# Kernel tuning notes

Measured on AMD Instinct MI355X. Metric: run time of the kernel, lower is better.

Reference implementation:

```python
import jax, jax.numpy as jnp
import numpy as np

PATCH_SIZES = (2, 4, 6, 8)
KERNEL_SIZES = (3, 5, 7)
K_FREQ = 1
K_ROUTE = 3


def setup_inputs():
    key = jax.random.key(0)
    ks = iter(jax.random.split(key, 40))
    B, T, N, D, dt = 8, 1024, 32, 128, 128
    P = len(PATCH_SIZES)
    def rn(shape, s=0.02):
        return jax.random.normal(next(ks), shape, jnp.float32) * s
    inp = {
        'z': jax.random.normal(next(ks), (B, T, N, D), jnp.float32),
        'noise_feat': jax.random.normal(next(ks), (B * N, T, D), jnp.float32),
        'noise_logits': jax.random.normal(next(ks), (B * N, T, P), jnp.float32),
        'Wq_tr': rn((D, len(KERNEL_SIZES))), 'bq_tr': jnp.zeros((len(KERNEL_SIZES),), jnp.float32),
        'Wf': rn((3 * D, D)), 'bf': jnp.zeros((D,), jnp.float32),
        'Wr': rn((D, P)), 'br': jnp.zeros((P,), jnp.float32),
        'Wn': rn((D, P)), 'bn': jnp.zeros((P,), jnp.float32),
        'local_qkv_w': rn((P, 3, D, dt)), 'local_qkv_b': jnp.zeros((P, 3, dt), jnp.float32),
        'gqkv_b': jnp.zeros((P, 3, dt), jnp.float32),
        'proj_w': rn((P, dt, D)), 'proj_b': jnp.zeros((P, D), jnp.float32),
        'conv_b': jnp.zeros((P, D), jnp.float32),
    }
    for p in PATCH_SIZES:
        inp['gqkv_w_p%d' % p] = rn((3, p * D, dt))
        inp['conv_w_p%d' % p] = rn((D, D, p))
    return inp


def _forward(z, noise_feat, noise_logits, Wq_tr, bq_tr, Wf, bf, Wr, br, Wn, bn,
             local_qkv_w, local_qkv_b, gqkv_w_p2, gqkv_w_p4, gqkv_w_p6, gqkv_w_p8,
             gqkv_b, proj_w, proj_b, conv_w_p2, conv_w_p4, conv_w_p6, conv_w_p8, conv_b):
    B, T, N, D = z.shape
    BN = B * N
    dt = proj_w.shape[1]
    P = len(PATCH_SIZES)
    zf = z.transpose(0, 2, 1, 3).reshape(BN, T, D)  # (BN, T, D)

    # --- DFT seasonal extractor: keep top-K_FREQ magnitude frequencies per (series, channel)
    zfft = jnp.fft.rfft(zf, axis=1)                 # (BN, F, D) complex
    mag = jnp.abs(zfft).astype(jnp.float32)
    Fr = mag.shape[1]
    magT = mag.transpose(0, 2, 1)                   # (BN, D, F)
    vals, idx = jax.lax.top_k(magT, K_FREQ)
    oh = (idx[..., None] == jnp.arange(Fr)).astype(jnp.float32)  # (BN, D, k, F)
    maskT = (oh * vals[..., None]).sum(axis=2)      # scatter top-k magnitudes
    factor = (maskT / (magT + 1e-8)).transpose(0, 2, 1)
    z_sea = jnp.fft.irfft(zfft * factor, n=T, axis=1).astype(zf.dtype)
    z_rem = zf - z_sea

    # --- multi-scale trend (avg_pool1d, count_include_pad=True, stride 1, pad k//2)
    alpha = jax.nn.softmax(z_rem.mean(axis=1) @ Wq_tr + bq_tr, axis=-1)  # (BN, n_k)
    def avg_pool(x, k):
        pd = k // 2
        xp = jnp.pad(x, ((0, 0), (pd, pd), (0, 0)))
        cs = jnp.pad(jnp.cumsum(xp, axis=1), ((0, 0), (1, 0), (0, 0)))
        return (cs[:, k:] - cs[:, :-k]) / k          # length T for odd k
    pooled = jnp.stack([avg_pool(z_rem, k) for k in KERNEL_SIZES], axis=1)  # (BN, n_k, T, D)
    z_trend = jnp.einsum('bk,bktd->btd', alpha, pooled)

    # --- noisy top-k gating router
    z_fused = jnp.concatenate([zf, z_sea, z_trend], axis=-1) @ Wf + bf
    gating = z_fused + noise_feat * 0.1
    logits = gating @ Wr + br + noise_logits * jax.nn.softplus(gating @ Wn + bn)
    rw = jax.nn.softmax(logits, axis=-1)            # (BN, T, P)
    tv, ti = jax.lax.top_k(rw, K_ROUTE)
    sparse = ((ti[..., None] == jnp.arange(P)).astype(rw.dtype) * tv[..., None]).sum(axis=2)

    # --- per-patch-size dual attention branches
    gqkv_ws = (gqkv_w_p2, gqkv_w_p4, gqkv_w_p6, gqkv_w_p8)
    conv_ws = (conv_w_p2, conv_w_p4, conv_w_p6, conv_w_p8)
    scale = dt ** -0.5
    out = jnp.zeros((BN, D, T), jnp.float32)
    for i, p in enumerate(PATCH_SIZES):
        pad = (-T) % p
        zp = jnp.pad(zf, ((0, 0), (0, pad), (0, 0)))
        Np = (T + pad) // p
        patches = zp.reshape(BN, Np, p, D)
        # local attention: patch-mean query against patch elements
        lw, lb = local_qkv_w[i], local_qkv_b[i]
        q = patches.mean(axis=2) @ lw[0] + lb[0]                   # (BN, Np, dt)
        kk = jnp.einsum('bnpd,de->bnpe', patches, lw[1]) + lb[1]
        vv = jnp.einsum('bnpd,de->bnpe', patches, lw[2]) + lb[2]
        la = jax.nn.softmax(jnp.einsum('bne,bnpe->bnp', q, kk) * scale, axis=-1)
        local_out = jnp.einsum('bnp,bnpe->bne', la, vv)
        # global attention over flattened patches (sigmoid THEN scale THEN softmax, as in source)
        flat = patches.reshape(BN, Np, p * D)
        gw, gb = gqkv_ws[i], gqkv_b[i]
        gq = flat @ gw[0] + gb[0]
        gk = flat @ gw[1] + gb[1]
        gv = flat @ gw[2] + gb[2]
        ga = jax.nn.softmax(jax.nn.sigmoid(jnp.einsum('bme,bne->bmn', gq, gk)) * scale, axis=-1)
        global_out = jnp.einsum('bmn,bne->bme', ga, gv)
        fused = (local_out + global_out) @ proj_w[i] + proj_b[i]   # (BN, Np, D)
        # ConvTranspose1d(kernel=stride=p): out[b,o,n*p+j] = sum_i fused[b,n,i] W[i,o,j] + bias
        up = (jnp.einsum('bni,ioj->bonj', fused, conv_ws[i]).reshape(BN, D, Np * p)
              + conv_b[i][None, :, None])[:, :, :T]
        out = out + up * sparse[:, :, i][:, None, :]
    # replicate original (BN, D, T) -> reshape(B, N, T, D) -> permute, exactly as source
    return out.reshape(B, N, T, D).transpose(0, 2, 1, 3)


def reference(z, noise_feat, noise_logits, Wq_tr, bq_tr, Wf, bf, Wr, br, Wn, bn,
              local_qkv_w, local_qkv_b, gqkv_w_p2, gqkv_w_p4, gqkv_w_p6, gqkv_w_p8,
              gqkv_b, proj_w, proj_b, conv_w_p2, conv_w_p4, conv_w_p6, conv_w_p8, conv_b):
    return _forward(z, noise_feat, noise_logits, Wq_tr, bq_tr, Wf, bf, Wr, br, Wn, bn,
                    local_qkv_w, local_qkv_b, gqkv_w_p2, gqkv_w_p4, gqkv_w_p6, gqkv_w_p8,
                    gqkv_b, proj_w, proj_b, conv_w_p2, conv_w_p4, conv_w_p6, conv_w_p8, conv_b)
```

## Files before the change

### kernel.cpp

```cpp
#include <hip/hip_runtime.h>
#include <math.h>

#define TID ((int)threadIdx.x)

static constexpr int Tn  = 1024;
static constexpr int Dn  = 128;
static constexpr int BNn = 256;
static constexpr long SL = 16777216;

typedef __attribute__((ext_vector_type(8))) short s16x8;
typedef __attribute__((ext_vector_type(4))) float f32x4;

__device__ __forceinline__ float wave_sum(float v) {
  v += __shfl_xor(v, 32); v += __shfl_xor(v, 16); v += __shfl_xor(v, 8);
  v += __shfl_xor(v, 4);  v += __shfl_xor(v, 2);  v += __shfl_xor(v, 1);
  return v;
}

__device__ __forceinline__ unsigned short f2bf(float f) {
  unsigned u = __float_as_uint(f);
  return (unsigned short)((u + 0x7FFFu + ((u >> 16) & 1u)) >> 16);
}
__device__ __forceinline__ float bf2f(unsigned short s) {
  return __uint_as_float(((unsigned)s) << 16);
}

__global__ __launch_bounds__(256) void transpose_k(const float* __restrict__ z, float* __restrict__ zf) {
  long g = (long)blockIdx.x * 256 + TID;
  int bn = (int)(g >> 15); int rem = (int)(g & 32767);
  int t = rem >> 5; int d4 = rem & 31;
  int b = bn >> 5, n = bn & 31;
  float4 v = ((const float4*)z)[(((long)b * Tn + t) * 32 + n) * 32 + d4];
  ((float4*)zf)[g] = v;
}

__global__ __launch_bounds__(256) void fft_k(const float* __restrict__ zf,
                                             int* __restrict__ keyf,
                                             float* __restrict__ amp_re, float* __restrict__ amp_im) {
  int bn = blockIdx.x;
  int d0 = blockIdx.y * 4;
  __shared__ float2 ctab[1024];
  __shared__ float zch[4][1024];
  __shared__ __align__(16) float Am[4][32][66];
  const float astep = 6.1359231515425649e-3f;
  for (int i = TID; i < 1024; i += 256) {
    float ang = (float)i * astep;
    ctab[i] = make_float2(cosf(ang), sinf(ang));
  }
  for (int t = TID; t < 1024; t += 256) {
    float4 v = *(const float4*)(zf + ((long)bn * Tn + t) * Dn + d0);
    zch[0][t] = v.x; zch[1][t] = v.y; zch[2][t] = v.z; zch[3][t] = v.w;
  }
  __syncthreads();
  int lane = TID & 63, wv = TID >> 6;
  int t0 = lane & 31, hi = lane >> 5;
  float zr[32];
  #pragma unroll
  for (int t1 = 0; t1 < 32; ++t1) zr[t1] = zch[wv][t0 + 32 * t1];
  for (int jj = 0; jj <= 8; ++jj) {
    int j = 2 * jj + hi;
    if (j <= 16) {
      float re = 0.f, im = 0.f;
      int stp = j << 5;
      int idx = 0;
      #pragma unroll
      for (int t1 = 0; t1 < 32; ++t1) {
        float2 w = ctab[idx];
        re += zr[t1] * w.x;
        im -= zr[t1] * w.y;
        idx = (idx + stp) & 1023;
      }
      *(float2*)&Am[wv][t0][2 * j] = make_float2(re, im);
      if (j >= 1 && j <= 15)
        *(float2*)&Am[wv][t0][2 * (32 - j)] = make_float2(re, -im);
    }
  }
  __syncthreads();
  unsigned long long bestkey = 0ULL;
  float bXR = 0.f, bXI = 0.f;
  for (int s = 0; s <= 8; ++s) {
    int k = lane + (s << 6);
    if (k <= 512) {
      int j = k & 31;
      float2 wk = ctab[k];
      float c = 1.f, sn = 0.f, XR = 0.f, XI = 0.f;
      #pragma unroll
      for (int tb = 0; tb < 32; ++tb) {
        float2 a = *(float2*)&Am[wv][tb][2 * j];
        XR += c * a.x + sn * a.y;
        XI += c * a.y - sn * a.x;
        float cn = c * wk.x - sn * wk.y;
        sn = sn * wk.x + c * wk.y;
        c = cn;
      }
      float m2 = XR * XR + XI * XI;
      unsigned long long key = ((unsigned long long)__float_as_uint(m2) << 32) | (unsigned)(1023 - k);
      if (key > bestkey) { bestkey = key; bXR = XR; bXI = XI; }
    }
  }
  #pragma unroll
  for (int off = 32; off >= 1; off >>= 1) {
    unsigned long long o = __shfl_xor(bestkey, off);
    if (o > bestkey) bestkey = o;
  }
  int fwin = 1023 - (int)(bestkey & 1023ULL);
  int owner = fwin & 63;
  float XRw = __shfl(bXR, owner);
  float XIw = __shfl(bXI, owner);
  if (lane == 0) {
    float mag = sqrtf(XRw * XRw + XIw * XIw);
    float factor = mag / (mag + 1e-8f);
    float w = (fwin == 0 || fwin == 512) ? 1.f : 2.f;
    float sc = w * (1.f / 1024.f) * factor;
    int d = d0 + wv;
    amp_re[bn * 128 + d] = XRw * sc;
    amp_im[bn * 128 + d] = XIw * sc;
    keyf[bn * 128 + d] = fwin;
  }
}

__global__ __launch_bounds__(256) void zrem_k(const float* __restrict__ zf,
                                              const int* __restrict__ keyf,
                                              const float* __restrict__ amp_re, const float* __restrict__ amp_im,
                                              float* __restrict__ z_rem) {
  __shared__ float tab[1024];
  for (int i = TID; i < 1024; i += 256) tab[i] = cosf((float)i * 6.1359231515425649e-3f);
  __syncthreads();
  long g = (long)blockIdx.x * 256 + TID;
  int bn = (int)(g >> 15); int rem = (int)(g & 32767);
  int t = rem >> 5; int d4 = (rem & 31) * 4;
  float4 zv = ((const float4*)zf)[g];
  float se[4];
  #pragma unroll
  for (int j = 0; j < 4; ++j) {
    int d = d4 + j;
    int f = keyf[bn * 128 + d];
    int idx = (f * t) & 1023;
    float cc = tab[idx], ss = tab[(idx + 768) & 1023];
    se[j] = amp_re[bn * 128 + d] * cc - amp_im[bn * 128 + d] * ss;
  }
  ((float4*)z_rem)[g] = make_float4(zv.x - se[0], zv.y - se[1], zv.z - se[2], zv.w - se[3]);
}

__global__ __launch_bounds__(256) void alpha_k(const float* __restrict__ z_rem,
                                               const float* __restrict__ Wq, const float* __restrict__ bq,
                                               float* __restrict__ alpha) {
  int bn = blockIdx.x;
  __shared__ float sm[128];
  __shared__ float lg[3];
  int d = TID & 127, half = TID >> 7;
  float s = 0.f;
  for (int t = half * 512; t < half * 512 + 512; ++t) s += z_rem[((long)bn * Tn + t) * Dn + d];
  if (!half) sm[d] = s;
  __syncthreads();
  if (half) sm[d] += s;
  __syncthreads();
  if (TID < 3) {
    float acc = 0.f;
    for (int dd = 0; dd < 128; ++dd) acc += sm[dd] * Wq[dd * 3 + TID];
    lg[TID] = acc * (1.f / 1024.f) + bq[TID];
  }
  __syncthreads();
  if (TID < 3) {
    float m = fmaxf(lg[0], fmaxf(lg[1], lg[2]));
    float e = expf(lg[TID] - m);
    float ssum = expf(lg[0] - m) + expf(lg[1] - m) + expf(lg[2] - m);
    alpha[bn * 3 + TID] = e / ssum;
  }
}

__global__ __launch_bounds__(256) void trend_k(const float* __restrict__ z_rem,
                                               const float* __restrict__ alpha, float* __restrict__ z_trend) {
  long g = (long)blockIdx.x * 256 + TID;
  int bn = (int)(g >> 15); int rem = (int)(g & 32767);
  int t = rem >> 5; int c4 = (rem & 31) * 4;
  float a0 = alpha[bn * 3 + 0], a1 = alpha[bn * 3 + 1], a2 = alpha[bn * 3 + 2];
  float w1 = a0 * (1.f / 3.f) + a1 * (1.f / 5.f) + a2 * (1.f / 7.f);
  float w2 = a1 * (1.f / 5.f) + a2 * (1.f / 7.f);
  float w3 = a2 * (1.f / 7.f);
  float wj[7] = {w3, w2, w1, w1, w1, w2, w3};
  float ax = 0.f, ay = 0.f, az = 0.f, aw = 0.f;
  #pragma unroll
  for (int j = -3; j <= 3; ++j) {
    int tt = t + j;
    if (tt < 0 || tt >= Tn) continue;
    float4 v = *(const float4*)(z_rem + ((long)bn * Tn + tt) * Dn + c4);
    float w = wj[j + 3];
    ax += w * v.x; ay += w * v.y; az += w * v.z; aw += w * v.w;
  }
  ((float4*)z_trend)[g] = make_float4(ax, ay, az, aw);
}

enum { GM_PLAIN = 0, GM_FLAT = 1, GM_PMEAN = 2 };

template<int MODE>
__device__ __forceinline__ float4 a_load4(const float* __restrict__ A, int r, int k, int K, int Np, int p) {
  if (MODE == GM_PLAIN) {
    return *(const float4*)(A + (long)r * K + k);
  } else if (MODE == GM_FLAT) {
    int bn = r / Np; int np_ = r - bn * Np;
    int t = np_ * p + (k >> 7);
    if (t < Tn) return *(const float4*)(A + ((long)bn * Tn + t) * Dn + (k & 127));
    return make_float4(0.f, 0.f, 0.f, 0.f);
  } else {
    int bn = r / Np; int np_ = r - bn * Np;
    int t0 = np_ * p;
    float4 sv = make_float4(0.f, 0.f, 0.f, 0.f);
    for (int j = 0; j < p; ++j) {
      int t = t0 + j;
      if (t < Tn) {
        float4 v = *(const float4*)(A + ((long)bn * Tn + t) * Dn + k);
        sv.x += v.x; sv.y += v.y; sv.z += v.z; sv.w += v.w;
      }
    }
    float inv = 1.f / (float)p;
    sv.x *= inv; sv.y *= inv; sv.z *= inv; sv.w *= inv;
    return sv;
  }
}

#define FMA_ROW(i, av) \
  acc[i][0] += (av) * bv.x; acc[i][1] += (av) * bv.y; acc[i][2] += (av) * bv.z; acc[i][3] += (av) * bv.w;

template<int MODE>
__global__ __launch_bounds__(256) void gemm_k(const float* __restrict__ A, const float* __restrict__ B,
                                              const float* __restrict__ bias, float* __restrict__ C,
                                              int M, int K, int ldb, int ldc, int Np, int p) {
  __shared__ float As[16][68];
  __shared__ float Bs[16][128];
  int r0 = blockIdx.x * 64;
  int colB = blockIdx.y * 128;
  float acc[8][4] = {{0}};
  int am = TID >> 2, ak = (TID & 3) * 4;
  int bk = TID >> 4, bc = (TID & 15) * 8;
  int tc = TID & 31, tr = TID >> 5;
  for (int k0 = 0; k0 < K; k0 += 16) {
    float4 av = a_load4<MODE>(A, r0 + am, k0 + ak, K, Np, p);
    float4 b0 = *(const float4*)(B + (long)(k0 + bk) * ldb + colB + bc);
    float4 b1 = *(const float4*)(B + (long)(k0 + bk) * ldb + colB + bc + 4);
    __syncthreads();
    As[ak + 0][am] = av.x; As[ak + 1][am] = av.y; As[ak + 2][am] = av.z; As[ak + 3][am] = av.w;
    *(float4*)&Bs[bk][bc] = b0; *(float4*)&Bs[bk][bc + 4] = b1;
    __syncthreads();
    #pragma unroll
    for (int kk = 0; kk < 16; ++kk) {
      float4 bv = *(float4*)&Bs[kk][tc * 4];
      float4 a0 = *(float4*)&As[kk][tr * 8];
      float4 a1 = *(float4*)&As[kk][tr * 8 + 4];
      FMA_ROW(0, a0.x) FMA_ROW(1, a0.y) FMA_ROW(2, a0.z) FMA_ROW(3, a0.w)
      FMA_ROW(4, a1.x) FMA_ROW(5, a1.y) FMA_ROW(6, a1.z) FMA_ROW(7, a1.w)
    }
  }
  float4 bb = make_float4(0.f, 0.f, 0.f, 0.f);
  if (bias) bb = *(const float4*)(bias + colB + tc * 4);
  #pragma unroll
  for (int i = 0; i < 8; ++i) {
    long r = r0 + tr * 8 + i;
    float4 o = make_float4(acc[i][0] + bb.x, acc[i][1] + bb.y, acc[i][2] + bb.z, acc[i][3] + bb.w);
    *(float4*)(C + r * (long)ldc + colB + tc * 4) = o;
  }
}

template<int MODE, int OUTB>
__global__ __launch_bounds__(256) void mgemm_k(const float* __restrict__ A,
                                               const unsigned short* __restrict__ BT,
                                               const float* __restrict__ bias, void* __restrict__ Cv,
                                               int M, int K, int ldc, int Np, int p) {
  __shared__ unsigned short As[128 * 72];
  __shared__ unsigned short Bs[128 * 72];
  int r0 = blockIdx.x * 128;
  int colB = blockIdx.y * 128;
  int wid = TID >> 6, lane = TID & 63;
  int wr = (wid >> 1) * 64, wc = (wid & 1) * 64;
  int l15 = lane & 15, l4 = lane >> 4;
  f32x4 acc[4][4];
  f32x4 zero4 = {0.f, 0.f, 0.f, 0.f};
  #pragma unroll
  for (int a = 0; a < 4; ++a)
    #pragma unroll
    for (int b = 0; b < 4; ++b) acc[a][b] = zero4;
  int sr = TID >> 1, sh = (TID & 1) * 32;
  for (int k0 = 0; k0 < K; k0 += 64) {
    float4 av[8];
    #pragma unroll
    for (int j = 0; j < 8; ++j) av[j] = a_load4<MODE>(A, r0 + sr, k0 + sh + 4 * j, K, Np, p);
    s16x8 bv[4];
    const unsigned short* bsrc = BT + (long)(colB + sr) * K + k0 + sh;
    #pragma unroll
    for (int j = 0; j < 4; ++j) bv[j] = *(const s16x8*)(bsrc + 8 * j);
    __syncthreads();
    unsigned short* ar = As + sr * 72 + sh;
    #pragma unroll
    for (int j = 0; j < 8; ++j) {
      unsigned long long w =
        (unsigned long long)f2bf(av[j].x) | ((unsigned long long)f2bf(av[j].y) << 16) |
        ((unsigned long long)f2bf(av[j].z) << 32) | ((unsigned long long)f2bf(av[j].w) << 48);
      *(unsigned long long*)(ar + 4 * j) = w;
    }
    unsigned short* brr = Bs + sr * 72 + sh;
    #pragma unroll
    for (int j = 0; j < 4; ++j) *(s16x8*)(brr + 8 * j) = bv[j];
    __syncthreads();
    #pragma unroll
    for (int kk = 0; kk < 2; ++kk) {
      int kb = kk * 32 + l4 * 8;
      s16x8 af[4], bfr[4];
      #pragma unroll
      for (int mf = 0; mf < 4; ++mf) af[mf] = *(s16x8*)(As + (wr + mf * 16 + l15) * 72 + kb);
      #pragma unroll
      for (int nf = 0; nf < 4; ++nf) bfr[nf] = *(s16x8*)(Bs + (wc + nf * 16 + l15) * 72 + kb);
      #pragma unroll
      for (int mf = 0; mf < 4; ++mf)
        #pragma unroll
        for (int nf = 0; nf < 4; ++nf)
          acc[mf][nf] = __builtin_amdgcn_mfma_f32_16x16x32_bf16(af[mf], bfr[nf], acc[mf][nf], 0, 0, 0);
    }
  }
  #pragma unroll
  for (int nf = 0; nf < 4; ++nf) {
    int col = colB + wc + nf * 16 + l15;
    float bb = bias ? bias[col] : 0.f;
    #pragma unroll
    for (int mf = 0; mf < 4; ++mf) {
      #pragma unroll
      for (int rg = 0; rg < 4; ++rg) {
        long row = r0 + wr + mf * 16 + l4 * 4 + rg;
        float v = acc[mf][nf][rg] + bb;
        if (OUTB) ((unsigned short*)Cv)[row * ldc + col] = f2bf(v);
        else      ((float*)Cv)[row * ldc + col] = v;
      }
    }
  }
}

__global__ __launch_bounds__(256) void makebt_k(const float* __restrict__ Wql, const float* __restrict__ lqkv_w,
                                                const float* __restrict__ g0, const float* __restrict__ g1,
                                                const float* __restrict__ g2, const float* __restrict__ g3,
                                                const float* __restrict__ proj_w,
                                                unsigned short* __restrict__ dst) {
  int ent = blockIdx.y; int i = ent / 6, e = ent - i * 6;
  const int PS[4] = {2, 4, 6, 8};
  const long BOFF[4] = {0, 147456, 393216, 737280};
  int p = PS[i];
  const float* gw = (i == 0) ? g0 : (i == 1) ? g1 : (i == 2) ? g2 : g3;
  const float* src; int K, N; long doff = BOFF[i];
  if (e == 0)      { src = Wql + (long)i * 16384;              K = 128;     N = 128; }
  else if (e == 1) { src = lqkv_w + (long)(i * 3 + 2) * 16384; K = 128;     N = 128; doff += 16384; }
  else if (e <= 4) { src = gw + (long)(e - 2) * p * 16384;     K = p * 128; N = 128; doff += 32768 + (long)(e - 2) * p * 16384; }
  else             { src = proj_w + (long)i * 16384;           K = 128;     N = 128; doff += 32768 + 3L * p * 16384; }
  long tot = (long)K * N;
  long idx = (long)blockIdx.x * 256 + TID;
  if (idx >= tot) return;
  int n = (int)(idx / K), k = (int)(idx - (long)n * K);
  dst[doff + idx] = f2bf(src[(long)k * N + n]);
}

__global__ __launch_bounds__(256) void router_k(const float* __restrict__ zf, const float* __restrict__ z_rem,
                                                const float* __restrict__ z_trend,
                                                const float* __restrict__ Wf, const float* __restrict__ bf,
                                                const float* __restrict__ nfeat, const float* __restrict__ nlog,
                                                const float* __restrict__ Wr, const float* __restrict__ br,
                                                const float* __restrict__ Wn, const float* __restrict__ bnb,
                                                float* __restrict__ sparse) {
  __shared__ float As[16][68];
  __shared__ float Bs[16][128];
  __shared__ float Cs[64][132];
  __shared__ float wrn[128][8];
  __shared__ float lrow[64][4];
  long r0 = (long)blockIdx.x * 64;
  float acc[8][4] = {{0}};
  int am = TID >> 2, ak = (TID & 3) * 4;
  int bk = TID >> 4, bc = (TID & 15) * 8;
  int tc = TID & 31, tr = TID >> 5;
  for (int k0 = 0; k0 < 384; k0 += 16) {
    int k = k0 + ak;
    long row = (r0 + am) * 128;
    float4 av;
    if (k < 128) {
      av = *(const float4*)(zf + row + k);
    } else if (k < 256) {
      float4 a = *(const float4*)(zf + row + (k - 128));
      float4 b = *(const float4*)(z_rem + row + (k - 128));
      av = make_float4(a.x - b.x, a.y - b.y, a.z - b.z, a.w - b.w);
    } else {
      av = *(const float4*)(z_trend + row + (k - 256));
    }
    float4 b0 = *(const float4*)(Wf + (long)(k0 + bk) * 128 + bc);
    float4 b1 = *(const float4*)(Wf + (long)(k0 + bk) * 128 + bc + 4);
    __syncthreads();
    As[ak + 0][am] = av.x; As[ak + 1][am] = av.y; As[ak + 2][am] = av.z; As[ak + 3][am] = av.w;
    *(float4*)&Bs[bk][bc] = b0; *(float4*)&Bs[bk][bc + 4] = b1;
    __syncthreads();
    #pragma unroll
    for (int kk = 0; kk < 16; ++kk) {
      float4 bv = *(float4*)&Bs[kk][tc * 4];
      float4 a0 = *(float4*)&As[kk][tr * 8];
      float4 a1 = *(float4*)&As[kk][tr * 8 + 4];
      FMA_ROW(0, a0.x) FMA_ROW(1, a0.y) FMA_ROW(2, a0.z) FMA_ROW(3, a0.w)
      FMA_ROW(4, a1.x) FMA_ROW(5, a1.y) FMA_ROW(6, a1.z) FMA_ROW(7, a1.w)
    }
  }
  for (int idx = TID; idx < 128; idx += 256) {
    #pragma unroll
    for (int c = 0; c < 4; ++c) { wrn[idx][c] = Wr[idx * 4 + c]; wrn[idx][4 + c] = Wn[idx * 4 + c]; }
  }
  #pragma unroll
  for (int i = 0; i < 8; ++i) {
    long r = r0 + tr * 8 + i;
    float4 nfv = *(const float4*)(nfeat + r * 128 + tc * 4);
    Cs[tr * 8 + i][tc * 4 + 0] = acc[i][0] + bf[tc * 4 + 0] + 0.1f * nfv.x;
    Cs[tr * 8 + i][tc * 4 + 1] = acc[i][1] + bf[tc * 4 + 1] + 0.1f * nfv.y;
    Cs[tr * 8 + i][tc * 4 + 2] = acc[i][2] + bf[tc * 4 + 2] + 0.1f * nfv.z;
    Cs[tr * 8 + i][tc * 4 + 3] = acc[i][3] + bf[tc * 4 + 3] + 0.1f * nfv.w;
  }
  __syncthreads();
  int rr = TID >> 2, c = TID & 3;
  float la = 0.f, lb2 = 0.f;
  for (int d = 0; d < 128; ++d) {
    float g = Cs[rr][d];
    la += g * wrn[d][c]; lb2 += g * wrn[d][4 + c];
  }
  long r = r0 + rr;
  float x = lb2 + bnb[c];
  float sp = (x > 0.f) ? x + log1pf(expf(-x)) : log1pf(expf(x));
  float lg = la + br[c] + nlog[r * 4 + c] * sp;
  lrow[rr][c] = lg;
  __syncthreads();
  float l0 = lrow[rr][0], l1 = lrow[rr][1], l2 = lrow[rr][2], l3 = lrow[rr][3];
  float mx = fmaxf(fmaxf(l0, l1), fmaxf(l2, l3));
  float e0 = expf(l0 - mx), e1 = expf(l1 - mx), e2 = expf(l2 - mx), e3 = expf(l3 - mx);
  float s = e0 + e1 + e2 + e3;
  float r0v = e0 / s, r1v = e1 / s, r2v = e2 / s, r3v = e3 / s;
  int zi = 0; float mv = r0v;
  if (r1v <= mv) { mv = r1v; zi = 1; }
  if (r2v <= mv) { mv = r2v; zi = 2; }
  if (r3v <= mv) { mv = r3v; zi = 3; }
  float rwc = (c == 0) ? r0v : (c == 1) ? r1v : (c == 2) ? r2v : r3v;
  sparse[r * 4 + c] = (c == zi) ? 0.f : rwc;
}

__global__ __launch_bounds__(256) void precompute_k(const float* __restrict__ lqkv_w,
                                                    const float* __restrict__ lqkv_b,
                                                    float* __restrict__ Wql, float* __restrict__ bql,
                                                    float* __restrict__ v1, float* __restrict__ c1) {
  int i = blockIdx.x;
  const float* lw0 = lqkv_w + (long)(i * 3 + 0) * 16384;
  const float* lw1 = lqkv_w + (long)(i * 3 + 1) * 16384;
  const float* lb0 = lqkv_b + (i * 3 + 0) * 128;
  const float* lb1 = lqkv_b + (i * 3 + 1) * 128;
  for (int idx = TID; idx < 16384; idx += 256) {
    int dp = idx >> 7, d = idx & 127;
    float s = 0.f;
    for (int e = 0; e < 128; ++e) s += lw0[dp * 128 + e] * lw1[d * 128 + e];
    Wql[(long)i * 16384 + idx] = s;
  }
  for (int d = TID; d < 128; d += 256) {
    float s = 0.f, s2 = 0.f;
    for (int e = 0; e < 128; ++e) { s += lb0[e] * lw1[d * 128 + e]; s2 += lw0[d * 128 + e] * lb1[e]; }
    bql[i * 128 + d] = s;
    v1[i * 128 + d] = s2;
  }
  if (TID == 0) {
    float s = 0.f;
    for (int e = 0; e < 128; ++e) s += lb0[e] * lb1[e];
    c1[i] = s;
  }
}

__global__ __launch_bounds__(256) void local_attn(const float* __restrict__ zf, const float* __restrict__ w_vec,
                                                  const float* __restrict__ v1, const float* __restrict__ c1,
                                                  float* __restrict__ pooled, int Np, int p, int ibr) {
  int lane = TID & 63, wid = TID >> 6;
  int r = blockIdx.x * 4 + wid;
  int bn = r / Np, np_ = r - bn * Np;
  int d0 = lane, d1 = lane + 64;
  float wv0 = w_vec[(long)r * 128 + d0];
  float wv1 = w_vec[(long)r * 128 + d1];
  float p0[8], p1[8], sj[8];
  #pragma unroll
  for (int j = 0; j < 8; ++j) {
    p0[j] = 0.f; p1[j] = 0.f;
    if (j < p) {
      int t = np_ * p + j;
      if (t < Tn) {
        const float* src = zf + ((long)bn * Tn + t) * Dn;
        p0[j] = src[d0]; p1[j] = src[d1];
      }
    }
    float v = wv0 * p0[j] + wv1 * p1[j];
    sj[j] = wave_sum(v);
  }
  float pm0 = 0.f, pm1 = 0.f;
  #pragma unroll
  for (int j = 0; j < 8; ++j) if (j < p) { pm0 += p0[j]; pm1 += p1[j]; }
  float invp = 1.f / (float)p;
  pm0 *= invp; pm1 *= invp;
  float qb = wave_sum(pm0 * v1[ibr * 128 + d0] + pm1 * v1[ibr * 128 + d1]) + c1[ibr];
  const float scale = 0.08838834764831845f;
  float mx = -1e30f;
  #pragma unroll
  for (int j = 0; j < 8; ++j) if (j < p) { sj[j] = (sj[j] + qb) * scale; mx = fmaxf(mx, sj[j]); }
  float se = 0.f; float ej[8];
  #pragma unroll
  for (int j = 0; j < 8; ++j) { ej[j] = 0.f; if (j < p) { ej[j] = expf(sj[j] - mx); se += ej[j]; } }
  float inv = 1.f / se;
  float o0 = 0.f, o1 = 0.f;
  #pragma unroll
  for (int j = 0; j < 8; ++j) if (j < p) { float w = ej[j] * inv; o0 += w * p0[j]; o1 += w * p1[j]; }
  pooled[(long)r * 128 + d0] = o0;
  pooled[(long)r * 128 + d1] = o1;
}

__global__ __launch_bounds__(256) void gattn_k(const unsigned short* __restrict__ gq,
                                               const unsigned short* __restrict__ gk,
                                               const unsigned short* __restrict__ gv,
                                               float* __restrict__ lo, int Np) {
  int mt = blockIdx.x, bn = blockIdx.y;
  int m0 = mt * 32;
  __shared__ float Q[32][132], Kt[32][132], Vt[32][132];
  __shared__ float W[32][36];
  __shared__ float denom[32];
  #pragma unroll
  for (int i = 0; i < 2; ++i) {
    int f8 = TID + 256 * i; int mm = f8 >> 4; int c8 = (f8 & 15) * 8;
    int m = m0 + mm;
    float4 q0 = make_float4(0.f, 0.f, 0.f, 0.f), q1 = q0;
    if (m < Np) {
      s16x8 qv = *(const s16x8*)(gq + ((long)bn * Np + m) * 128 + c8);
      q0 = make_float4(bf2f((unsigned short)qv[0]), bf2f((unsigned short)qv[1]),
                       bf2f((unsigned short)qv[2]), bf2f((unsigned short)qv[3]));
      q1 = make_float4(bf2f((unsigned short)qv[4]), bf2f((unsigned short)qv[5]),
                       bf2f((unsigned short)qv[6]), bf2f((unsigned short)qv[7]));
    }
    *(float4*)&Q[mm][c8] = q0; *(float4*)&Q[mm][c8 + 4] = q1;
  }
  if (TID < 32) denom[TID] = 0.f;
  float4 ac0 = make_float4(0.f, 0.f, 0.f, 0.f), ac1 = ac0, ac2 = ac0, ac3 = ac0;
  int mmS = TID >> 3, nb = TID & 7;
  int mb = TID >> 5, e4 = (TID & 31) * 4;
  const float scale = 0.08838834764831845f;
  for (int n0 = 0; n0 < Np; n0 += 32) {
    __syncthreads();
    #pragma unroll
    for (int i = 0; i < 2; ++i) {
      int f8 = TID + 256 * i; int nn = f8 >> 4; int c8 = (f8 & 15) * 8;
      int n = n0 + nn;
      float4 k0v = make_float4(0.f, 0.f, 0.f, 0.f), k1v = k0v, v0v = k0v, v1v = k0v;
      if (n < Np) {
        s16x8 kv = *(const s16x8*)(gk + ((long)bn * Np + n) * 128 + c8);
        s16x8 vv = *(const s16x8*)(gv + ((long)bn * Np + n) * 128 + c8);
        k0v = make_float4(bf2f((unsigned short)kv[0]), bf2f((unsigned short)kv[1]),
                          bf2f((unsigned short)kv[2]), bf2f((unsigned short)kv[3]));
        k1v = make_float4(bf2f((unsigned short)kv[4]), bf2f((unsigned short)kv[5]),
                          bf2f((unsigned short)kv[6]), bf2f((unsigned short)kv[7]));
        v0v = make_float4(bf2f((unsigned short)vv[0]), bf2f((unsigned short)vv[1]),
                          bf2f((unsigned short)vv[2]), bf2f((unsigned short)vv[3]));
        v1v = make_float4(bf2f((unsigned short)vv[4]), bf2f((unsigned short)vv[5]),
                          bf2f((unsigned short)vv[6]), bf2f((unsigned short)vv[7]));
      }
      *(float4*)&Kt[nn][c8] = k0v; *(float4*)&Kt[nn][c8 + 4] = k1v;
      *(float4*)&Vt[nn][c8] = v0v; *(float4*)&Vt[nn][c8 + 4] = v1v;
    }
    __syncthreads();
    float s0 = 0.f, s1 = 0.f, s2 = 0.f, s3 = 0.f;
    #pragma unroll 8
    for (int e = 0; e < 128; e += 4) {
      float4 q4 = *(float4*)&Q[mmS][e];
      float4 k0 = *(float4*)&Kt[nb + 0][e];
      float4 k1 = *(float4*)&Kt[nb + 8][e];
      float4 k2 = *(float4*)&Kt[nb + 16][e];
      float4 k3 = *(float4*)&Kt[nb + 24][e];
      s0 += q4.x * k0.x + q4.y * k0.y + q4.z * k0.z + q4.w * k0.w;
      s1 += q4.x * k1.x + q4.y * k1.y + q4.z * k1.z + q4.w * k1.w;
      s2 += q4.x * k2.x + q4.y * k2.y + q4.z * k2.z + q4.w * k2.w;
      s3 += q4.x * k3.x + q4.y * k3.y + q4.z * k3.z + q4.w * k3.w;
    }
    float sv[4] = {s0, s1, s2, s3};
    #pragma unroll
    for (int u = 0; u < 4; ++u) {
      int n = n0 + nb + 8 * u;
      float w = 0.f;
      if (n < Np) {
        float sg = 1.f / (1.f + expf(-sv[u]));
        w = expf(sg * scale);
      }
      W[mmS][nb + 8 * u] = w;
    }
    __syncthreads();
    if (TID < 32) {
      float dsum = 0.f;
      for (int nn = 0; nn < 32; ++nn) dsum += W[TID][nn];
      denom[TID] += dsum;
    }
    #pragma unroll 4
    for (int nn = 0; nn < 32; ++nn) {
      float4 v4 = *(float4*)&Vt[nn][e4];
      float w0 = W[mb][nn], w1 = W[mb + 8][nn], w2 = W[mb + 16][nn], w3 = W[mb + 24][nn];
      ac0.x += w0 * v4.x; ac0.y += w0 * v4.y; ac0.z += w0 * v4.z; ac0.w += w0 * v4.w;
      ac1.x += w1 * v4.x; ac1.y += w1 * v4.y; ac1.z += w1 * v4.z; ac1.w += w1 * v4.w;
      ac2.x += w2 * v4.x; ac2.y += w2 * v4.y; ac2.z += w2 * v4.z; ac2.w += w2 * v4.w;
      ac3.x += w3 * v4.x; ac3.y += w3 * v4.y; ac3.z += w3 * v4.z; ac3.w += w3 * v4.w;
    }
  }
  __syncthreads();
  #pragma unroll
  for (int kk2 = 0; kk2 < 4; ++kk2) {
    int m = m0 + mb + 8 * kk2;
    if (m < Np) {
      float inv = 1.f / denom[mb + 8 * kk2];
      float* lp = lo + ((long)bn * Np + m) * 128 + e4;
      float4 cur = *(float4*)lp;
      float4 a = (kk2 == 0) ? ac0 : (kk2 == 1) ? ac1 : (kk2 == 2) ? ac2 : ac3;
      cur.x += a.x * inv; cur.y += a.y * inv; cur.z += a.z * inv; cur.w += a.w * inv;
      *(float4*)lp = cur;
    }
  }
}

__global__ __launch_bounds__(256) void scatter2_k(const float* __restrict__ up_t, const float* __restrict__ sparse,
                                                  const float* __restrict__ cb, float* __restrict__ out,
                                                  int Np, int p, int ibr) {
  int bn = blockIdx.x; int t0 = blockIdx.y * 128; int o0 = blockIdx.z * 16;
  __shared__ float tile[16][132];
  int np0 = t0 / p;
  int np1 = (t0 + 127) / p;
  if (np1 > Np - 1) np1 = Np - 1;
  int per = 16 * p;
  int npi = 256 / per;
  int sub = TID / per;
  int e   = TID - sub * per;
  int ol = e / p, j = e - ol * p;
  for (int npb = np0; npb <= np1; npb += npi) {
    int np_ = npb + sub;
    if (sub < npi && np_ <= np1) {
      int t = np_ * p + j;
      if (t >= t0 && t < t0 + 128 && t < Tn) {
        tile[ol][t - t0] = up_t[(((long)bn * Np + np_) * 128 + o0 + ol) * (long)p + j];
      }
    }
  }
  __syncthreads();
  int dd = TID & 127, ow = TID >> 7;
  int t = t0 + dd;
  float sp = sparse[((long)bn * 1024 + t) * 4 + ibr];
  int b = bn >> 5, n = bn & 31;
  int thi = t0 >> 7;
  for (int ol2 = ow; ol2 < 16; ol2 += 2) {
    int o = o0 + ol2;
    float v = sp * (tile[ol2][dd] + cb[o]);
    long idx = (((long)b * 1024 + o * 8 + thi) * 32 + n) * 128 + dd;
    out[idx] += v;
  }
}

extern "C" void kernel_launch(void* const* d_in, const int* in_sizes, int n_in,
                              void* d_out, int out_size, void* d_ws, size_t ws_size,
                              hipStream_t stream) {
  const float* z      = (const float*)d_in[0];
  const float* nfeat  = (const float*)d_in[1];
  const float* nlog   = (const float*)d_in[2];
  const float* Wq_tr  = (const float*)d_in[3];
  const float* bq_tr  = (const float*)d_in[4];
  const float* Wf     = (const float*)d_in[5];
  const float* bf     = (const float*)d_in[6];
  const float* Wr     = (const float*)d_in[7];
  const float* br     = (const float*)d_in[8];
  const float* Wn     = (const float*)d_in[9];
  const float* bnb    = (const float*)d_in[10];
  const float* lqkv_w = (const float*)d_in[11];
  const float* lqkv_b = (const float*)d_in[12];
  const float* gqkvb  = (const float*)d_in[13];
  const float* proj_w = (const float*)d_in[14];
  const float* proj_b = (const float*)d_in[15];
  const float* conv_b = (const float*)d_in[16];
  const float* gqkv_w[4] = {(const float*)d_in[17], (const float*)d_in[19],
                            (const float*)d_in[21], (const float*)d_in[23]};
  const float* conv_w[4] = {(const float*)d_in[18], (const float*)d_in[20],
                            (const float*)d_in[22], (const float*)d_in[24]};
  float* out = (float*)d_out;
  float* ws = (float*)d_ws;

  float* zf     = ws;
  float* LOOP   = ws + 2 * SL;
  float* sparse = ws + 6 * SL;
  int*   keyf   = (int*)(sparse + 1048576);
  float* amp_re = sparse + 1048576 + 65536;
  float* amp_im = amp_re + 32768;
  float* alpha  = amp_im + 32768;
  float* Wql    = alpha + 1024;
  float* bql    = Wql + 65536;
  float* v1     = bql + 512;
  float* c1     = v1 + 512;
  unsigned short* BT = (unsigned short*)(ws + 5 * SL + SL / 2);

  float* z_rem   = LOOP;
  float* z_trend = LOOP + 2 * SL;

  hipMemsetAsync(out, 0, (size_t)out_size * sizeof(float), stream);

  transpose_k<<<32768, 256, 0, stream>>>(z, zf);
  fft_k<<<dim3(256, 32), 256, 0, stream>>>(zf, keyf, amp_re, amp_im);
  zrem_k<<<32768, 256, 0, stream>>>(zf, keyf, amp_re, amp_im, z_rem);
  alpha_k<<<256, 256, 0, stream>>>(z_rem, Wq_tr, bq_tr, alpha);
  trend_k<<<32768, 256, 0, stream>>>(z_rem, alpha, z_trend);
  router_k<<<4096, 256, 0, stream>>>(zf, z_rem, z_trend, Wf, bf, nfeat, nlog, Wr, br, Wn, bnb, sparse);
  precompute_k<<<4, 256, 0, stream>>>(lqkv_w, lqkv_b, Wql, bql, v1, c1);
  makebt_k<<<dim3(512, 24), 256, 0, stream>>>(Wql, lqkv_w, gqkv_w[0], gqkv_w[1], gqkv_w[2], gqkv_w[3],
                                              proj_w, BT);

  const int PS[4]   = {2, 4, 6, 8};
  const int NPs[4]  = {512, 256, 171, 128};
  const long BOFF[4] = {0, 147456, 393216, 737280};
  for (int i = 0; i < 4; ++i) {
    int p = PS[i], Np = NPs[i];
    int M = BNn * Np;
    float* w_vec  = LOOP + 0 * SL;
    float* pooled = LOOP + 1 * SL;
    float* lob    = LOOP + 2 * SL;
    unsigned short* gqb = (unsigned short*)(LOOP + 0 * SL);
    unsigned short* gkb = (unsigned short*)(LOOP + 1 * SL);
    unsigned short* gvb = (unsigned short*)(LOOP + 3 * SL);
    float* fusedb = LOOP + 0 * SL;
    float* up_t   = LOOP + 1 * SL;

    long bo = BOFF[i];
    const unsigned short* bt_wql  = BT + bo;
    const unsigned short* bt_lv   = BT + bo + 16384;
    const unsigned short* bt_g0   = BT + bo + 32768;
    const unsigned short* bt_g1   = bt_g0 + (long)p * 16384;
    const unsigned short* bt_g2   = bt_g1 + (long)p * 16384;
    const unsigned short* bt_proj = bt_g0 + 3L * p * 16384;

    mgemm_k<GM_PMEAN, 0><<<dim3(M / 128, 1), 256, 0, stream>>>(zf, bt_wql, bql + i * 128,
                                                               w_vec, M, 128, 128, Np, p);
    local_attn<<<M / 4, 256, 0, stream>>>(zf, w_vec, v1, c1, pooled, Np, p, i);
    mgemm_k<GM_PLAIN, 0><<<dim3(M / 128, 1), 256, 0, stream>>>(pooled, bt_lv, lqkv_b + (i * 3 + 2) * 128,
                                                               lob, M, 128, 128, Np, p);
    mgemm_k<GM_FLAT, 1><<<dim3(M / 128, 1), 256, 0, stream>>>(zf, bt_g0, gqkvb + (i * 3 + 0) * 128,
                                                              gqb, M, p * 128, 128, Np, p);
    mgemm_k<GM_FLAT, 1><<<dim3(M / 128, 1), 256, 0, stream>>>(zf, bt_g1, gqkvb + (i * 3 + 1) * 128,
                                                              gkb, M, p * 128, 128, Np, p);
    mgemm_k<GM_FLAT, 1><<<dim3(M / 128, 1), 256, 0, stream>>>(zf, bt_g2, gqkvb + (i * 3 + 2) * 128,
                                                              gvb, M, p * 128, 128, Np, p);
    gattn_k<<<dim3((Np + 31) / 32, 256), 256, 0, stream>>>(gqb, gkb, gvb, lob, Np);
    mgemm_k<GM_PLAIN, 0><<<dim3(M / 128, 1), 256, 0, stream>>>(lob, bt_proj, proj_b + i * 128,
                                                               fusedb, M, 128, 128, Np, p);
    gemm_k<GM_PLAIN><<<dim3(M / 64, p), 256, 0, stream>>>(fusedb, conv_w[i], nullptr, up_t,
                                                          M, 128, 128 * p, 128 * p, Np, p);
    scatter2_k<<<dim3(256, 8, 8), 256, 0, stream>>>(up_t, sparse, conv_b + i * 128, out, Np, p, i);
  }
}
```

Before: 5.322 ms.

## Move global attention and transposed-conv GEMM onto bf16 MFMA paths

Rewrites the global sigmoid-softmax attention as an MFMA kernel. Q·K scores and the weighted sum over V now use bf16 matrix instructions, and the V projection writes a transposed, zero-padded bf16 layout so it can be fed directly as an MFMA operand. The fp32 SIMT transposed-conv GEMM is replaced by the bf16 MFMA GEMM, with conv weights pre-transposed into the bf16 weight buffer. This removes scalar-FMA compute bottlenecks at the cost of lower precision in the attention weights and conv, plus an extra memset for padded Np.

```diff
diff --git a/kernel.cpp b/kernel.cpp
--- a/kernel.cpp
+++ b/kernel.cpp
@@ -222,45 +222,6 @@
 #define FMA_ROW(i, av) \
   acc[i][0] += (av) * bv.x; acc[i][1] += (av) * bv.y; acc[i][2] += (av) * bv.z; acc[i][3] += (av) * bv.w;
 
-template<int MODE>
-__global__ __launch_bounds__(256) void gemm_k(const float* __restrict__ A, const float* __restrict__ B,
-                                              const float* __restrict__ bias, float* __restrict__ C,
-                                              int M, int K, int ldb, int ldc, int Np, int p) {
-  __shared__ float As[16][68];
-  __shared__ float Bs[16][128];
-  int r0 = blockIdx.x * 64;
-  int colB = blockIdx.y * 128;
-  float acc[8][4] = {{0}};
-  int am = TID >> 2, ak = (TID & 3) * 4;
-  int bk = TID >> 4, bc = (TID & 15) * 8;
-  int tc = TID & 31, tr = TID >> 5;
-  for (int k0 = 0; k0 < K; k0 += 16) {
-    float4 av = a_load4<MODE>(A, r0 + am, k0 + ak, K, Np, p);
-    float4 b0 = *(const float4*)(B + (long)(k0 + bk) * ldb + colB + bc);
-    float4 b1 = *(const float4*)(B + (long)(k0 + bk) * ldb + colB + bc + 4);
-    __syncthreads();
-    As[ak + 0][am] = av.x; As[ak + 1][am] = av.y; As[ak + 2][am] = av.z; As[ak + 3][am] = av.w;
-    *(float4*)&Bs[bk][bc] = b0; *(float4*)&Bs[bk][bc + 4] = b1;
-    __syncthreads();
-    #pragma unroll
-    for (int kk = 0; kk < 16; ++kk) {
-      float4 bv = *(float4*)&Bs[kk][tc * 4];
-      float4 a0 = *(float4*)&As[kk][tr * 8];
-      float4 a1 = *(float4*)&As[kk][tr * 8 + 4];
-      FMA_ROW(0, a0.x) FMA_ROW(1, a0.y) FMA_ROW(2, a0.z) FMA_ROW(3, a0.w)
-      FMA_ROW(4, a1.x) FMA_ROW(5, a1.y) FMA_ROW(6, a1.z) FMA_ROW(7, a1.w)
-    }
-  }
-  float4 bb = make_float4(0.f, 0.f, 0.f, 0.f);
-  if (bias) bb = *(const float4*)(bias + colB + tc * 4);
-  #pragma unroll
-  for (int i = 0; i < 8; ++i) {
-    long r = r0 + tr * 8 + i;
-    float4 o = make_float4(acc[i][0] + bb.x, acc[i][1] + bb.y, acc[i][2] + bb.z, acc[i][3] + bb.w);
-    *(float4*)(C + r * (long)ldc + colB + tc * 4) = o;
-  }
-}
-
 template<int MODE, int OUTB>
 __global__ __launch_bounds__(256) void mgemm_k(const float* __restrict__ A,
                                                const unsigned short* __restrict__ BT,
@@ -324,10 +285,16 @@
     for (int mf = 0; mf < 4; ++mf) {
       #pragma unroll
       for (int rg = 0; rg < 4; ++rg) {
-        long row = r0 + wr + mf * 16 + l4 * 4 + rg;
+        int row = r0 + wr + mf * 16 + l4 * 4 + rg;
         float v = acc[mf][nf][rg] + bb;
-        if (OUTB) ((unsigned short*)Cv)[row * ldc + col] = f2bf(v);
-        else      ((float*)Cv)[row * ldc + col] = v;
+        if (OUTB == 1) {
+          ((unsigned short*)Cv)[(long)row * ldc + col] = f2bf(v);
+        } else if (OUTB == 2) {
+          int bnr = row / Np; int np_ = row - bnr * Np;
+          ((unsigned short*)Cv)[((long)bnr * 128 + col) * ldc + np_] = f2bf(v);
+        } else {
+          ((float*)Cv)[(long)row * ldc + col] = v;
+        }
       }
     }
   }
@@ -337,17 +304,21 @@
                                                 const float* __restrict__ g0, const float* __restrict__ g1,
                                                 const float* __restrict__ g2, const float* __restrict__ g3,
                                                 const float* __restrict__ proj_w,
+                                                const float* __restrict__ c0, const float* __restrict__ c1w,
+                                                const float* __restrict__ c2, const float* __restrict__ c3,
                                                 unsigned short* __restrict__ dst) {
-  int ent = blockIdx.y; int i = ent / 6, e = ent - i * 6;
+  int ent = blockIdx.y; int i = ent / 7, e = ent - i * 7;
   const int PS[4] = {2, 4, 6, 8};
-  const long BOFF[4] = {0, 147456, 393216, 737280};
+  const long BOFF[4] = {0, 180224, 491520, 933888};
   int p = PS[i];
   const float* gw = (i == 0) ? g0 : (i == 1) ? g1 : (i == 2) ? g2 : g3;
+  const float* cw = (i == 0) ? c0 : (i == 1) ? c1w : (i == 2) ? c2 : c3;
   const float* src; int K, N; long doff = BOFF[i];
   if (e == 0)      { src = Wql + (long)i * 16384;              K = 128;     N = 128; }
   else if (e == 1) { src = lqkv_w + (long)(i * 3 + 2) * 16384; K = 128;     N = 128; doff += 16384; }
   else if (e <= 4) { src = gw + (long)(e - 2) * p * 16384;     K = p * 128; N = 128; doff += 32768 + (long)(e - 2) * p * 16384; }
-  else             { src = proj_w + (long)i * 16384;           K = 128;     N = 128; doff += 32768 + 3L * p * 16384; }
+  else if (e == 5) { src = proj_w + (long)i * 16384;           K = 128;     N = 128; doff += 32768 + 3L * p * 16384; }
+  else             { src = cw;                                 K = 128;     N = 128 * p; doff += 49152 + 3L * p * 16384; }
   long tot = (long)K * N;
   long idx = (long)blockIdx.x * 256 + TID;
   if (idx >= tot) return;
@@ -511,108 +482,80 @@
   pooled[(long)r * 128 + d1] = o1;
 }
 
-__global__ __launch_bounds__(256) void gattn_k(const unsigned short* __restrict__ gq,
+__global__ __launch_bounds__(256) void gattn_m(const unsigned short* __restrict__ gq,
                                                const unsigned short* __restrict__ gk,
-                                               const unsigned short* __restrict__ gv,
-                                               float* __restrict__ lo, int Np) {
-  int mt = blockIdx.x, bn = blockIdx.y;
-  int m0 = mt * 32;
-  __shared__ float Q[32][132], Kt[32][132], Vt[32][132];
-  __shared__ float W[32][36];
-  __shared__ float denom[32];
-  #pragma unroll
-  for (int i = 0; i < 2; ++i) {
-    int f8 = TID + 256 * i; int mm = f8 >> 4; int c8 = (f8 & 15) * 8;
-    int m = m0 + mm;
-    float4 q0 = make_float4(0.f, 0.f, 0.f, 0.f), q1 = q0;
+                                               const unsigned short* __restrict__ gvT,
+                                               float* __restrict__ lo, int Np, int NpT) {
+  int bn = blockIdx.y;
+  int q0 = blockIdx.x * 64;
+  int wid = TID >> 6, lane = TID & 63;
+  int l15 = lane & 15, l4 = lane >> 4;
+  __shared__ __align__(16) unsigned short Wl[4][16][40];
+  const float scale = 0.08838834764831845f;
+
+  int qrow = q0 + 16 * wid + l15;
+  const unsigned short* qbase = gq + ((long)bn * Np + min(qrow, Np - 1)) * 128 + l4 * 8;
+  s16x8 aq[4];
+  #pragma unroll
+  for (int c = 0; c < 4; ++c) aq[c] = *(const s16x8*)(qbase + c * 32);
+
+  f32x4 z4 = {0.f, 0.f, 0.f, 0.f};
+  f32x4 outa[8];
+  #pragma unroll
+  for (int dsb = 0; dsb < 8; ++dsb) outa[dsb] = z4;
+  float dsum[4] = {0.f, 0.f, 0.f, 0.f};
+
+  int ntiles = (Np + 31) >> 5;
+  for (int nt = 0; nt < ntiles; ++nt) {
+    int n0 = nt * 32;
+    f32x4 sacc[2];
+    sacc[0] = z4; sacc[1] = z4;
+    #pragma unroll
+    for (int st = 0; st < 2; ++st) {
+      int nrow = n0 + st * 16 + l15;
+      const unsigned short* kbase = gk + ((long)bn * Np + min(nrow, Np - 1)) * 128 + l4 * 8;
+      #pragma unroll
+      for (int c = 0; c < 4; ++c) {
+        s16x8 bk = *(const s16x8*)(kbase + c * 32);
+        sacc[st] = __builtin_amdgcn_mfma_f32_16x16x32_bf16(aq[c], bk, sacc[st], 0, 0, 0);
+      }
+    }
+    #pragma unroll
+    for (int st = 0; st < 2; ++st) {
+      int n = n0 + st * 16 + l15;
+      bool ok = (n < Np);
+      #pragma unroll
+      for (int r = 0; r < 4; ++r) {
+        float s = sacc[st][r];
+        float sg = __builtin_amdgcn_rcpf(1.f + __expf(-s));
+        float w = ok ? __expf(scale * sg) : 0.f;
+        unsigned short wb = f2bf(w);
+        dsum[r] += ok ? bf2f(wb) : 0.f;
+        Wl[wid][l4 * 4 + r][st * 16 + l15] = wb;
+      }
+    }
+    s16x8 aw = *(s16x8*)&Wl[wid][l15][l4 * 8];
+    const unsigned short* vbase = gvT + ((long)bn * 128 + l15) * NpT + n0 + l4 * 8;
+    #pragma unroll
+    for (int dsb = 0; dsb < 8; ++dsb) {
+      s16x8 bv = *(const s16x8*)(vbase + (long)dsb * 16 * NpT);
+      outa[dsb] = __builtin_amdgcn_mfma_f32_16x16x32_bf16(aw, bv, outa[dsb], 0, 0, 0);
+    }
+  }
+  float inv[4];
+  #pragma unroll
+  for (int r = 0; r < 4; ++r) {
+    float v = dsum[r];
+    v += __shfl_xor(v, 1); v += __shfl_xor(v, 2); v += __shfl_xor(v, 4); v += __shfl_xor(v, 8);
+    inv[r] = 1.f / v;
+  }
+  #pragma unroll
+  for (int r = 0; r < 4; ++r) {
+    int m = q0 + 16 * wid + l4 * 4 + r;
     if (m < Np) {
-      s16x8 qv = *(const s16x8*)(gq + ((long)bn * Np + m) * 128 + c8);
-      q0 = make_float4(bf2f((unsigned short)qv[0]), bf2f((unsigned short)qv[1]),
-                       bf2f((unsigned short)qv[2]), bf2f((unsigned short)qv[3]));
-      q1 = make_float4(bf2f((unsigned short)qv[4]), bf2f((unsigned short)qv[5]),
-                       bf2f((unsigned short)qv[6]), bf2f((unsigned short)qv[7]));
-    }
-    *(float4*)&Q[mm][c8] = q0; *(float4*)&Q[mm][c8 + 4] = q1;
-  }
-  if (TID < 32) denom[TID] = 0.f;
-  float4 ac0 = make_float4(0.f, 0.f, 0.f, 0.f), ac1 = ac0, ac2 = ac0, ac3 = ac0;
-  int mmS = TID >> 3, nb = TID & 7;
-  int mb = TID >> 5, e4 = (TID & 31) * 4;
-  const float scale = 0.08838834764831845f;
-  for (int n0 = 0; n0 < Np; n0 += 32) {
-    __syncthreads();
-    #pragma unroll
-    for (int i = 0; i < 2; ++i) {
-      int f8 = TID + 256 * i; int nn = f8 >> 4; int c8 = (f8 & 15) * 8;
-      int n = n0 + nn;
-      float4 k0v = make_float4(0.f, 0.f, 0.f, 0.f), k1v = k0v, v0v = k0v, v1v = k0v;
-      if (n < Np) {
-        s16x8 kv = *(const s16x8*)(gk + ((long)bn * Np + n) * 128 + c8);
-        s16x8 vv = *(const s16x8*)(gv + ((long)bn * Np + n) * 128 + c8);
-        k0v = make_float4(bf2f((unsigned short)kv[0]), bf2f((unsigned short)kv[1]),
-                          bf2f((unsigned short)kv[2]), bf2f((unsigned short)kv[3]));
-        k1v = make_float4(bf2f((unsigned short)kv[4]), bf2f((unsigned short)kv[5]),
-                          bf2f((unsigned short)kv[6]), bf2f((unsigned short)kv[7]));
-        v0v = make_float4(bf2f((unsigned short)vv[0]), bf2f((unsigned short)vv[1]),
-                          bf2f((unsigned short)vv[2]), bf2f((unsigned short)vv[3]));
-        v1v = make_float4(bf2f((unsigned short)vv[4]), bf2f((unsigned short)vv[5]),
-                          bf2f((unsigned short)vv[6]), bf2f((unsigned short)vv[7]));
-      }
-      *(float4*)&Kt[nn][c8] = k0v; *(float4*)&Kt[nn][c8 + 4] = k1v;
-      *(float4*)&Vt[nn][c8] = v0v; *(float4*)&Vt[nn][c8 + 4] = v1v;
-    }
-    __syncthreads();
-    float s0 = 0.f, s1 = 0.f, s2 = 0.f, s3 = 0.f;
-    #pragma unroll 8
-    for (int e = 0; e < 128; e += 4) {
-      float4 q4 = *(float4*)&Q[mmS][e];
-      float4 k0 = *(float4*)&Kt[nb + 0][e];
-      float4 k1 = *(float4*)&Kt[nb + 8][e];
-      float4 k2 = *(float4*)&Kt[nb + 16][e];
-      float4 k3 = *(float4*)&Kt[nb + 24][e];
-      s0 += q4.x * k0.x + q4.y * k0.y + q4.z * k0.z + q4.w * k0.w;
-      s1 += q4.x * k1.x + q4.y * k1.y + q4.z * k1.z + q4.w * k1.w;
-      s2 += q4.x * k2.x + q4.y * k2.y + q4.z * k2.z + q4.w * k2.w;
-      s3 += q4.x * k3.x + q4.y * k3.y + q4.z * k3.z + q4.w * k3.w;
-    }
-    float sv[4] = {s0, s1, s2, s3};
-    #pragma unroll
-    for (int u = 0; u < 4; ++u) {
-      int n = n0 + nb + 8 * u;
-      float w = 0.f;
-      if (n < Np) {
-        float sg = 1.f / (1.f + expf(-sv[u]));
-        w = expf(sg * scale);
-      }
-      W[mmS][nb + 8 * u] = w;
-    }
-    __syncthreads();
-    if (TID < 32) {
-      float dsum = 0.f;
-      for (int nn = 0; nn < 32; ++nn) dsum += W[TID][nn];
-      denom[TID] += dsum;
-    }
-    #pragma unroll 4
-    for (int nn = 0; nn < 32; ++nn) {
-      float4 v4 = *(float4*)&Vt[nn][e4];
-      float w0 = W[mb][nn], w1 = W[mb + 8][nn], w2 = W[mb + 16][nn], w3 = W[mb + 24][nn];
-      ac0.x += w0 * v4.x; ac0.y += w0 * v4.y; ac0.z += w0 * v4.z; ac0.w += w0 * v4.w;
-      ac1.x += w1 * v4.x; ac1.y += w1 * v4.y; ac1.z += w1 * v4.z; ac1.w += w1 * v4.w;
-      ac2.x += w2 * v4.x; ac2.y += w2 * v4.y; ac2.z += w2 * v4.z; ac2.w += w2 * v4.w;
-      ac3.x += w3 * v4.x; ac3.y += w3 * v4.y; ac3.z += w3 * v4.z; ac3.w += w3 * v4.w;
-    }
-  }
-  __syncthreads();
-  #pragma unroll
-  for (int kk2 = 0; kk2 < 4; ++kk2) {
-    int m = m0 + mb + 8 * kk2;
-    if (m < Np) {
-      float inv = 1.f / denom[mb + 8 * kk2];
-      float* lp = lo + ((long)bn * Np + m) * 128 + e4;
-      float4 cur = *(float4*)lp;
-      float4 a = (kk2 == 0) ? ac0 : (kk2 == 1) ? ac1 : (kk2 == 2) ? ac2 : ac3;
-      cur.x += a.x * inv; cur.y += a.y * inv; cur.z += a.z * inv; cur.w += a.w * inv;
-      *(float4*)lp = cur;
+      float* lp = lo + ((long)bn * Np + m) * 128 + l15;
+      #pragma unroll
+      for (int dsb = 0; dsb < 8; ++dsb) lp[dsb * 16] += outa[dsb][r] * inv[r];
     }
   }
 }
@@ -705,21 +648,22 @@
   trend_k<<<32768, 256, 0, stream>>>(z_rem, alpha, z_trend);
   router_k<<<4096, 256, 0, stream>>>(zf, z_rem, z_trend, Wf, bf, nfeat, nlog, Wr, br, Wn, bnb, sparse);
   precompute_k<<<4, 256, 0, stream>>>(lqkv_w, lqkv_b, Wql, bql, v1, c1);
-  makebt_k<<<dim3(512, 24), 256, 0, stream>>>(Wql, lqkv_w, gqkv_w[0], gqkv_w[1], gqkv_w[2], gqkv_w[3],
-                                              proj_w, BT);
+  makebt_k<<<dim3(512, 28), 256, 0, stream>>>(Wql, lqkv_w, gqkv_w[0], gqkv_w[1], gqkv_w[2], gqkv_w[3],
+                                              proj_w, conv_w[0], conv_w[1], conv_w[2], conv_w[3], BT);
 
   const int PS[4]   = {2, 4, 6, 8};
   const int NPs[4]  = {512, 256, 171, 128};
-  const long BOFF[4] = {0, 147456, 393216, 737280};
+  const int NPTs[4] = {512, 256, 192, 128};
+  const long BOFF[4] = {0, 180224, 491520, 933888};
   for (int i = 0; i < 4; ++i) {
-    int p = PS[i], Np = NPs[i];
+    int p = PS[i], Np = NPs[i], NpT = NPTs[i];
     int M = BNn * Np;
     float* w_vec  = LOOP + 0 * SL;
     float* pooled = LOOP + 1 * SL;
     float* lob    = LOOP + 2 * SL;
     unsigned short* gqb = (unsigned short*)(LOOP + 0 * SL);
     unsigned short* gkb = (unsigned short*)(LOOP + 1 * SL);
-    unsigned short* gvb = (unsigned short*)(LOOP + 3 * SL);
+    unsigned short* gvT = (unsigned short*)(LOOP + 3 * SL);
     float* fusedb = LOOP + 0 * SL;
     float* up_t   = LOOP + 1 * SL;
 
@@ -730,6 +674,7 @@
     const unsigned short* bt_g1   = bt_g0 + (long)p * 16384;
     const unsigned short* bt_g2   = bt_g1 + (long)p * 16384;
     const unsigned short* bt_proj = bt_g0 + 3L * p * 16384;
+    const unsigned short* bt_conv = bt_proj + 16384;
 
     mgemm_k<GM_PMEAN, 0><<<dim3(M / 128, 1), 256, 0, stream>>>(zf, bt_wql, bql + i * 128,
                                                                w_vec, M, 128, 128, Np, p);
@@ -740,13 +685,15 @@
                                                               gqb, M, p * 128, 128, Np, p);
     mgemm_k<GM_FLAT, 1><<<dim3(M / 128, 1), 256, 0, stream>>>(zf, bt_g1, gqkvb + (i * 3 + 1) * 128,
                                                               gkb, M, p * 128, 128, Np, p);
-    mgemm_k<GM_FLAT, 1><<<dim3(M / 128, 1), 256, 0, stream>>>(zf, bt_g2, gqkvb + (i * 3 + 2) * 128,
-                                                              gvb, M, p * 128, 128, Np, p);
-    gattn_k<<<dim3((Np + 31) / 32, 256), 256, 0, stream>>>(gqb, gkb, gvb, lob, Np);
+    if (NpT != Np)
+      hipMemsetAsync((void*)gvT, 0, (size_t)256 * 128 * NpT * 2, stream);
+    mgemm_k<GM_FLAT, 2><<<dim3(M / 128, 1), 256, 0, stream>>>(zf, bt_g2, gqkvb + (i * 3 + 2) * 128,
+                                                              gvT, M, p * 128, NpT, Np, p);
+    gattn_m<<<dim3((Np + 63) / 64, 256), 256, 0, stream>>>(gqb, gkb, gvT, lob, Np, NpT);
     mgemm_k<GM_PLAIN, 0><<<dim3(M / 128, 1), 256, 0, stream>>>(lob, bt_proj, proj_b + i * 128,
                                                                fusedb, M, 128, 128, Np, p);
-    gemm_k<GM_PLAIN><<<dim3(M / 64, p), 256, 0, stream>>>(fusedb, conv_w[i], nullptr, up_t,
-                                                          M, 128, 128 * p, 128 * p, Np, p);
+    mgemm_k<GM_PLAIN, 0><<<dim3(M / 128, p), 256, 0, stream>>>(fusedb, bt_conv, nullptr, up_t,
+                                                               M, 128, 128 * p, Np, p);
     scatter2_k<<<dim3(256, 8, 8), 256, 0, stream>>>(up_t, sparse, conv_b + i * 128, out, Np, p, i);
   }
 }
```

Measured after the change: 4.284 ms. 19.5% less time.
